# Kernel optimization log

Hardware: AMD Instinct MI355X
Metric: run time of the kernel (lower is better)

Reference implementation:

```python
import jax, jax.numpy as jnp
import numpy as np
import math

D_MODEL = 1024
N_HEADS = 16
HEAD_DIM = D_MODEL // N_HEADS
MLP_DIM = 4 * D_MODEL
B, L, M = 2, 2048, 2048


def layer_norm(x, g, b, eps=1e-5):
    mu = jnp.mean(x, axis=-1, keepdims=True)
    var = jnp.var(x, axis=-1, keepdims=True)
    return (x - mu) * jax.lax.rsqrt(var + eps) * g + b


def mha(q_in, k_in, qW, wW, oW, mask=None):
    # Faithful to source: k and v share w_proj, and the value einsum uses k.
    b, l, _ = q_in.shape
    m = k_in.shape[1]
    q = (q_in @ qW).reshape(b, l, HEAD_DIM, N_HEADS)
    k = (k_in @ wW).reshape(b, m, HEAD_DIM, N_HEADS)
    s = jnp.einsum('bldn,bmdn->blmn', q, k)
    if mask is not None:
        s = jnp.where(mask, -1e9, s)  # mask applied BEFORE scaling, as in source
    s = s / math.sqrt(HEAD_DIM)
    w = jax.nn.softmax(s, axis=2)
    x = jnp.einsum('blmn,bmdn->bldn', w, k)  # source bug: uses k, not v
    x = x.reshape(b, l, HEAD_DIM * N_HEADS)
    return x @ oW


def setup_inputs() -> dict:
    key = jax.random.key(0)
    ks = jax.random.split(key, 16)
    sc = 1.0 / math.sqrt(D_MODEL)
    inp = {
        'x': jax.random.normal(ks[0], (B, L, D_MODEL), jnp.float32),
        'enc_output': jax.random.normal(ks[1], (B, M, D_MODEL), jnp.float32),
        'mask': jax.random.randint(ks[2], (B, 1, M, 1), 0, 2).astype(bool),
        'q1W': jax.random.normal(ks[3], (D_MODEL, D_MODEL), jnp.float32) * sc,
        'w1W': jax.random.normal(ks[4], (D_MODEL, D_MODEL), jnp.float32) * sc,
        'o1W': jax.random.normal(ks[5], (D_MODEL, D_MODEL), jnp.float32) * sc,
        'q2W': jax.random.normal(ks[6], (D_MODEL, D_MODEL), jnp.float32) * sc,
        'w2W': jax.random.normal(ks[7], (D_MODEL, D_MODEL), jnp.float32) * sc,
        'o2W': jax.random.normal(ks[8], (D_MODEL, D_MODEL), jnp.float32) * sc,
        'ffW1': jax.random.normal(ks[9], (D_MODEL, MLP_DIM), jnp.float32) * sc,
        'ffb1': jnp.zeros((MLP_DIM,), jnp.float32),
        'ffW2': jax.random.normal(ks[10], (MLP_DIM, D_MODEL), jnp.float32) * sc,
        'ffb2': jnp.zeros((D_MODEL,), jnp.float32),
        'g1': jnp.ones((D_MODEL,), jnp.float32), 'b1': jnp.zeros((D_MODEL,), jnp.float32),
        'g2': jnp.ones((D_MODEL,), jnp.float32), 'b2': jnp.zeros((D_MODEL,), jnp.float32),
        'g3': jnp.ones((D_MODEL,), jnp.float32), 'b3': jnp.zeros((D_MODEL,), jnp.float32),
    }
    return inp


def reference(x, enc_output, mask, q1W, w1W, o1W, q2W, w2W, o2W,
              ffW1, ffb1, ffW2, ffb2, g1, b1, g2, b2, g3, b3):
    # self-attention (no mask, as in source)
    sa = mha(x, x, q1W, w1W, o1W, mask=None)
    x = layer_norm(x + sa, g1, b1)
    # encoder-decoder attention with mask
    ca = mha(x, enc_output, q2W, w2W, o2W, mask=mask)
    x = layer_norm(x + ca, g2, b2)
    # feed-forward (exact GELU, matching torch nn.GELU default)
    h = jax.nn.gelu(x @ ffW1 + ffb1, approximate=False)
    ff = h @ ffW2 + ffb2
    x = layer_norm(x + ff, g3, b3)
    return x
```

## Files before the change

### kernel.cpp

```cpp
#include <hip/hip_runtime.h>
#include <hip/hip_bf16.h>
#include <math.h>
#include <stdint.h>

typedef __attribute__((ext_vector_type(8))) short bf16x8_t;
typedef __attribute__((ext_vector_type(4))) float f32x4_t;

#define LOG2E 1.4426950408889634f
#define GLB(p) ((const __attribute__((address_space(1))) void*)(p))
#define LDS(p) ((__attribute__((address_space(3))) void*)(p))

__device__ __forceinline__ unsigned short f2bf(float f) {
    union { float f; unsigned int u; } v; v.f = f;
    unsigned int r = v.u + 0x7FFFu + ((v.u >> 16) & 1u);
    return (unsigned short)(r >> 16);
}

__device__ __forceinline__ float bf2f(unsigned short us) {
    union { unsigned int u; float f; } c; c.u = (unsigned int)us << 16; return c.f;
}

__device__ __forceinline__ unsigned int pack2bf(float a, float b) {
#if __has_builtin(__builtin_amdgcn_cvt_pk_bf16_f32)
    auto r = __builtin_amdgcn_cvt_pk_bf16_f32(a, b);
    unsigned int u;
    __builtin_memcpy(&u, &r, 4);
    return u;
#else
    return (unsigned int)f2bf(a) | ((unsigned int)f2bf(b) << 16);
#endif
}

__device__ __forceinline__ float fast_rcp(float x) {
#if __has_builtin(__builtin_amdgcn_rcpf)
    return __builtin_amdgcn_rcpf(x);
#else
    return 1.0f / x;
#endif
}

__device__ __forceinline__ float fexp2(float x) {
#if __has_builtin(__builtin_amdgcn_exp2f)
    return __builtin_amdgcn_exp2f(x);
#else
    return exp2f(x);
#endif
}

__device__ __forceinline__ float gelu_fast(float v) {
    float x2 = v * v;
    float inner = v * fmaf(0.0356774081f, x2, 0.7978845608f);
    inner = fminf(fmaxf(inner, -20.f), 20.f);
    float t = fexp2(inner * 2.8853900817779268f);
    return v * t * fast_rcp(t + 1.0f);
}

__global__ void cast2_bf16_k(const float* __restrict__ inA, unsigned short* __restrict__ outA,
                             const float* __restrict__ inB, unsigned short* __restrict__ outB,
                             int n4, const int* __restrict__ maskp, float* __restrict__ mask4) {
    if (blockIdx.y == 2) {
        int i = blockIdx.x * blockDim.x + threadIdx.x;
        if (i < 8192) {
            int nt = i & 3, l16 = (i >> 2) & 15, t = (i >> 6) & 31, b = (i >> 11) & 1;
            mask4[i] = maskp[b * 2048 + t * 64 + nt * 16 + l16] ? -1e10f : 0.0f;
        }
        return;
    }
    const float* in = blockIdx.y ? inB : inA;
    unsigned short* out = blockIdx.y ? outB : outA;
    int i = blockIdx.x * blockDim.x + threadIdx.x;
    if (i < n4) {
        float4 v = ((const float4*)in)[i];
        ushort4 o;
        o.x = f2bf(v.x); o.y = f2bf(v.y); o.z = f2bf(v.z); o.w = f2bf(v.w);
        ((ushort4*)out)[i] = o;
    }
}

__global__ void transpose_all_k(const float* __restrict__ s0, const float* __restrict__ s1,
                                const float* __restrict__ s2, const float* __restrict__ s3,
                                const float* __restrict__ s4, const float* __restrict__ s5,
                                const float* __restrict__ s6, const float* __restrict__ s7,
                                unsigned short* __restrict__ d0, unsigned short* __restrict__ d1,
                                unsigned short* __restrict__ d2, unsigned short* __restrict__ d3,
                                unsigned short* __restrict__ d4, unsigned short* __restrict__ d5,
                                unsigned short* __restrict__ d6, unsigned short* __restrict__ d7) {
    __shared__ float tile[32][33];
    int idx = blockIdx.x;
    const float* W; unsigned short* Wt; int K, N, bx, by;
    if (idx < 6144) {
        int which = idx >> 10, t = idx & 1023;
        bx = t & 31; by = t >> 5; K = 1024; N = 1024;
        switch (which) {
            case 0: W = s0; Wt = d0; break;
            case 1: W = s1; Wt = d1; break;
            case 2: W = s2; Wt = d2; break;
            case 3: W = s3; Wt = d3; break;
            case 4: W = s4; Wt = d4; break;
            default: W = s5; Wt = d5; break;
        }
    } else if (idx < 10240) {
        int t = idx - 6144;
        bx = t & 127; by = t >> 7; K = 1024; N = 4096;
        W = s6; Wt = d6;
    } else {
        int t = idx - 10240;
        bx = t & 31; by = t >> 5; K = 4096; N = 1024;
        W = s7; Wt = d7;
    }
    int k0 = by * 32, n0 = bx * 32;
    int tx = threadIdx.x, ty = threadIdx.y;
#pragma unroll
    for (int i = 0; i < 32; i += 8)
        tile[ty + i][tx] = W[(long)(k0 + ty + i) * N + n0 + tx];
    __syncthreads();
#pragma unroll
    for (int i = 0; i < 32; i += 8)
        Wt[(long)(n0 + ty + i) * K + k0 + tx] = f2bf(tile[tx][ty + i]);
}

template <int EP, int BN>
__global__ __launch_bounds__(256) void gemm_k(const unsigned short* __restrict__ A,
                                              const unsigned short* __restrict__ Bt,
                                              void* __restrict__ outp,
                                              const float* __restrict__ bias,
                                              int M, int N, int K) {
    __shared__ __align__(16) unsigned short As[128 * 64];
    __shared__ __align__(16) unsigned short Bs[BN * 64];
    const int NT = BN / 32;
    const int BG = BN / 32;
    int tid = threadIdx.x;
    int wave = tid >> 6, lane = tid & 63;
    int wm = wave >> 1, wn = wave & 1;
    int quad = lane >> 4, l16 = lane & 15;
    int bm = blockIdx.y * 128, bn = blockIdx.x * BN;

    f32x4_t acc[4][NT] = {};

    int srow = tid >> 3;
    int sgrp = (tid & 7) ^ (srow & 7);
    const unsigned short* Ag[4];
#pragma unroll
    for (int i = 0; i < 4; i++)
        Ag[i] = A + (long)(bm + i * 32 + srow) * K + sgrp * 8;
    const unsigned short* Bg[BG];
#pragma unroll
    for (int i = 0; i < BG; i++)
        Bg[i] = Bt + (long)(bn + i * 32 + srow) * K + sgrp * 8;

    for (int k0 = 0; k0 < K; k0 += 64) {
        __syncthreads();
#pragma unroll
        for (int i = 0; i < 4; i++)
            __builtin_amdgcn_global_load_lds(GLB(Ag[i] + k0), LDS(As + i * 2048 + tid * 8), 16, 0, 0);
#pragma unroll
        for (int i = 0; i < BG; i++)
            __builtin_amdgcn_global_load_lds(GLB(Bg[i] + k0), LDS(Bs + i * 2048 + tid * 8), 16, 0, 0);
        __syncthreads();
#pragma unroll
        for (int kk = 0; kk < 2; kk++) {
            int xg = ((kk * 4 + quad) ^ (l16 & 7)) * 8;
            bf16x8_t af[4], bfr[NT];
#pragma unroll
            for (int t = 0; t < 4; t++)
                af[t] = *(const bf16x8_t*)(As + (wm * 64 + t * 16 + l16) * 64 + xg);
#pragma unroll
            for (int t = 0; t < NT; t++)
                bfr[t] = *(const bf16x8_t*)(Bs + (wn * (BN / 2) + t * 16 + l16) * 64 + xg);
#pragma unroll
            for (int mt = 0; mt < 4; mt++)
#pragma unroll
                for (int nt = 0; nt < NT; nt++)
                    acc[mt][nt] = __builtin_amdgcn_mfma_f32_16x16x32_bf16(af[mt], bfr[nt], acc[mt][nt], 0, 0, 0);
        }
    }

#pragma unroll
    for (int mt = 0; mt < 4; mt++)
#pragma unroll
        for (int nt = 0; nt < NT; nt++)
#pragma unroll
            for (int r = 0; r < 4; r++) {
                int gm = bm + wm * 64 + mt * 16 + quad * 4 + r;
                int gn = bn + wn * (BN / 2) + nt * 16 + l16;
                float v = acc[mt][nt][r];
                if (EP == 2) {
                    v = gelu_fast(v + bias[gn]);
                    ((unsigned short*)outp)[(long)gm * N + gn] = f2bf(v);
                } else {
                    ((unsigned short*)outp)[(long)gm * N + gn] = f2bf(v);
                }
            }
}

template <int EP>
__global__ __launch_bounds__(512, 4) void gemm8_k(const unsigned short* __restrict__ A,
                                                  const unsigned short* __restrict__ Bt,
                                                  void* __restrict__ outp,
                                                  const float* __restrict__ bias,
                                                  const unsigned short* __restrict__ A2,
                                                  const unsigned short* __restrict__ Bt2,
                                                  unsigned short* __restrict__ qout,
                                                  unsigned short* __restrict__ kout,
                                                  unsigned short* __restrict__ ktout,
                                                  int M, int N, int K) {
    if (blockIdx.z) { A = A2; Bt = Bt2; }
    __shared__ __align__(16) unsigned short SMEM[32768];
    unsigned short* As = SMEM;
    unsigned short* Bs = SMEM + 16384;
    int tid = threadIdx.x;
    int wave = tid >> 6, lane = tid & 63;
    int wm = wave >> 2, wn = wave & 3;
    int quad = lane >> 4, l16 = lane & 15;
    int bm = blockIdx.y * 128, bn = blockIdx.x * 128;

    f32x4_t acc[4][2] = {};

    int srow = tid >> 3;
    int sgrp = (tid & 7) ^ (srow & 7);
    const unsigned short* Ag[2];
    const unsigned short* Bg[2];
#pragma unroll
    for (int i = 0; i < 2; i++) {
        Ag[i] = A + (long)(bm + i * 64 + srow) * K + sgrp * 8;
        Bg[i] = Bt + (long)(bn + i * 64 + srow) * K + sgrp * 8;
    }

    auto stage = [&](int buf, int k0) {
#pragma unroll
        for (int i = 0; i < 2; i++)
            __builtin_amdgcn_global_load_lds(GLB(Ag[i] + k0), LDS(As + buf * 8192 + i * 4096 + tid * 8), 16, 0, 0);
#pragma unroll
        for (int i = 0; i < 2; i++)
            __builtin_amdgcn_global_load_lds(GLB(Bg[i] + k0), LDS(Bs + buf * 8192 + i * 4096 + tid * 8), 16, 0, 0);
    };

    auto compute = [&](int buf) {
        const unsigned short* Ab = As + buf * 8192;
        const unsigned short* Bb = Bs + buf * 8192;
#pragma unroll
        for (int kk = 0; kk < 2; kk++) {
            int xg = ((kk * 4 + quad) ^ (l16 & 7)) * 8;
            bf16x8_t af[4], bfr[2];
#pragma unroll
            for (int t = 0; t < 4; t++)
                af[t] = *(const bf16x8_t*)(Ab + (wm * 64 + t * 16 + l16) * 64 + xg);
#pragma unroll
            for (int t = 0; t < 2; t++)
                bfr[t] = *(const bf16x8_t*)(Bb + (wn * 32 + t * 16 + l16) * 64 + xg);
#pragma unroll
            for (int mt = 0; mt < 4; mt++)
#pragma unroll
                for (int nt = 0; nt < 2; nt++)
                    acc[mt][nt] = __builtin_amdgcn_mfma_f32_16x16x32_bf16(af[mt], bfr[nt], acc[mt][nt], 0, 0, 0);
        }
    };

    stage(0, 0);
    const int NS = K >> 6;
    for (int i = 0; i < NS; i++) {
        if (i + 1 < NS) {
            stage((i + 1) & 1, (i + 1) << 6);
            asm volatile("s_waitcnt vmcnt(4)\n\ts_barrier" ::: "memory");
        } else {
            asm volatile("s_waitcnt vmcnt(0)\n\ts_barrier" ::: "memory");
        }
        compute(i & 1);
        asm volatile("s_barrier" ::: "memory");
    }

    if (EP == 7 || EP == 8) {
        bool kmode = (EP == 7) ? (bn >= 1024) : (blockIdx.z != 0);
        int G = (EP == 7 && kmode) ? ((bn - 1024) >> 7) : (bn >> 7);
        unsigned short* Ct = SMEM;
#pragma unroll
        for (int mt = 0; mt < 4; mt++)
#pragma unroll
            for (int nt = 0; nt < 2; nt++)
#pragma unroll
                for (int r = 0; r < 4; r++) {
                    int rr = wm * 64 + mt * 16 + quad * 4 + r;
                    int cc = wn * 32 + nt * 16 + l16;
                    Ct[rr * 132 + cc] = f2bf(acc[mt][nt][r]);
                }
        __syncthreads();
        int bq = bm >> 11;
        if (!kmode) {
#pragma unroll
            for (int i = 0; i < 4; i++) {
                int e = tid + i * 512;
                int h = e & 15, rl = e >> 4;
                int ll = (bm & 2047) + rl;
                union { uint4 v; unsigned short s[8]; } u;
#pragma unroll
                for (int j = 0; j < 8; j++) u.s[j] = Ct[rl * 132 + j * 16 + h];
                *(uint4*)(qout + (((long)(bq * 16 + h) * 2048 + ll) << 6) + ((G ^ (ll & 7)) << 3)) = u.v;
            }
        } else {
#pragma unroll
            for (int i = 0; i < 4; i++) {
                int e = tid + i * 512;
                int h = e & 15, rl = e >> 4;
                int mm = (bm & 2047) + rl;
                union { uint4 v; unsigned short s[8]; } u;
#pragma unroll
                for (int j = 0; j < 8; j++) u.s[j] = Ct[rl * 132 + j * 16 + h];
                *(uint4*)(kout + (((long)(bq * 16 + h) * 2048 + mm) << 6) + ((G ^ (mm & 7)) << 3)) = u.v;
            }
#pragma unroll
            for (int i = 0; i < 4; i++) {
                int e = tid + i * 512;
                int glog = e & 7, m0s = (e >> 3) & 1, dl = (e >> 4) & 7, h = e >> 7;
                int d = G * 8 + dl;
                union { uint4 v; unsigned short s[8]; } u;
#pragma unroll
                for (int j = 0; j < 8; j++) {
                    int p = glog * 8 + j;
                    int ml = (p >> 2) + (p & 3) * 16;
                    u.s[j] = Ct[(m0s * 64 + ml) * 132 + dl * 16 + h];
                }
                int mmbase = (bm & 2047) + m0s * 64;
                int gph = glog ^ (d & 7);
                *(uint4*)(ktout + ((long)(bq * 16 + h) * 64 + d) * 2048 + mmbase + gph * 8) = u.v;
            }
        }
        return;
    }

#pragma unroll
    for (int mt = 0; mt < 4; mt++)
#pragma unroll
        for (int nt = 0; nt < 2; nt++)
#pragma unroll
            for (int r = 0; r < 4; r++) {
                int gm = bm + wm * 64 + mt * 16 + quad * 4 + r;
                int gn = bn + wn * 32 + nt * 16 + l16;
                float v = acc[mt][nt][r];
                if (EP == 6) {
                    ((unsigned short*)outp)[(long)gm * N + gn] = f2bf(v + bias[gn]);
                } else {
                    ((unsigned short*)outp)[(long)gm * N + gn] = f2bf(v);
                }
            }
}

template <int USE_MASK>
__global__ __launch_bounds__(256, 4) void flash_attn9_k(const unsigned short* __restrict__ Qh,
                                                        const unsigned short* __restrict__ Kh,
                                                        const unsigned short* __restrict__ KhTp,
                                                        const float* __restrict__ mask4,
                                                        unsigned short* __restrict__ out) {
    __shared__ __align__(16) unsigned short K1[64 * 64];
    __shared__ __align__(16) unsigned short K2[64 * 64];
    __shared__ __align__(16) unsigned short Ps[64 * 64];
    __shared__ __align__(16) float Ml[USE_MASK ? 2048 : 4];

    int tid = threadIdx.x;
    int wave = tid >> 6, lane = tid & 63;
    int quad = lane >> 4, l16 = lane & 15;
    int bh = blockIdx.y, b = bh >> 4, h = bh & 15;
    int l0 = blockIdx.x * 64;
    const unsigned short* k1p = Kh + (long)bh * 2048 * 64 + tid * 8;
    const unsigned short* k2p = KhTp + (long)bh * 64 * 2048 + (long)(tid >> 3) * 2048 + (tid & 7) * 8;

    int sw = l16 & 7;

    const unsigned short* qrow = Qh + ((long)bh * 2048 + l0 + wave * 16 + l16) * 64;
    bf16x8_t qf[2];
#pragma unroll
    for (int kk = 0; kk < 2; kk++)
        qf[kk] = *(const bf16x8_t*)(qrow + ((kk * 4 + quad) ^ sw) * 8);

    __builtin_amdgcn_global_load_lds(GLB(k1p), LDS(K1 + tid * 8), 16, 0, 0);
    __builtin_amdgcn_global_load_lds(GLB(k1p + 2048), LDS(K1 + tid * 8 + 2048), 16, 0, 0);
    __builtin_amdgcn_global_load_lds(GLB(k2p), LDS(K2 + tid * 8), 16, 0, 0);
    __builtin_amdgcn_global_load_lds(GLB(k2p + 32 * 2048), LDS(K2 + tid * 8 + 2048), 16, 0, 0);
    if (USE_MASK) {
        const float* mp = mask4 + b * 2048;
        for (int c = tid; c < 512; c += 256)
            ((float4*)Ml)[c] = ((const float4*)mp)[c];
    }
    __syncthreads();

    const float C1 = 0.125f * LOG2E;
    f32x4_t acc_o[4] = {};
    float rs[4] = {0.f, 0.f, 0.f, 0.f};

    for (int t = 0; t < 32; ++t) {
        uint4 rA, rB, rC, rD;
        if (t < 31) {
            k1p += 4096;
            k2p += 64;
            rA = *(const uint4*)(k1p);
            rB = *(const uint4*)(k1p + 2048);
            rC = *(const uint4*)(k2p);
            rD = *(const uint4*)(k2p + 32 * 2048);
        }

        float4 mq = make_float4(0.f, 0.f, 0.f, 0.f);
        if (USE_MASK) mq = *(const float4*)(Ml + t * 64 + l16 * 4);

        f32x4_t sacc[4] = {};
        __builtin_amdgcn_s_setprio(1);
#pragma unroll
        for (int kk = 0; kk < 2; kk++) {
            int xg = ((kk * 4 + quad) ^ sw) * 8;
#pragma unroll
            for (int nt = 0; nt < 4; nt++) {
                bf16x8_t bfr = *(const bf16x8_t*)(K1 + (nt * 16 + l16) * 64 + xg);
                sacc[nt] = __builtin_amdgcn_mfma_f32_16x16x32_bf16(qf[kk], bfr, sacc[nt], 0, 0, 0);
            }
        }
        __builtin_amdgcn_s_setprio(0);

#pragma unroll
        for (int r = 0; r < 4; r++) {
            float p0 = fexp2(fmaf(sacc[0][r], C1, mq.x));
            float p1 = fexp2(fmaf(sacc[1][r], C1, mq.y));
            float p2 = fexp2(fmaf(sacc[2][r], C1, mq.z));
            float p3 = fexp2(fmaf(sacc[3][r], C1, mq.w));
            rs[r] += (p0 + p1) + (p2 + p3);
            uint2 pk; pk.x = pack2bf(p0, p1); pk.y = pack2bf(p2, p3);
            int Rrow = wave * 16 + quad * 4 + r;
            int grp = (l16 >> 1) ^ (Rrow & 7);
            *(uint2*)(Ps + Rrow * 64 + grp * 8 + (l16 & 1) * 4) = pk;
        }

        __builtin_amdgcn_s_setprio(1);
#pragma unroll
        for (int kk = 0; kk < 2; kk++) {
            int xg = ((kk * 4 + quad) ^ sw) * 8;
            int Rr = wave * 16 + l16;
            int pg = ((kk * 4 + quad) ^ (l16 & 7)) * 8;
            bf16x8_t af = *(const bf16x8_t*)(Ps + Rr * 64 + pg);
#pragma unroll
            for (int nt = 0; nt < 4; nt++) {
                bf16x8_t bfr = *(const bf16x8_t*)(K2 + (nt * 16 + l16) * 64 + xg);
                acc_o[nt] = __builtin_amdgcn_mfma_f32_16x16x32_bf16(af, bfr, acc_o[nt], 0, 0, 0);
            }
        }
        __builtin_amdgcn_s_setprio(0);

        asm volatile("s_barrier" ::: "memory");
        if (t < 31) {
            *(uint4*)(K1 + tid * 8) = rA;
            *(uint4*)(K1 + tid * 8 + 2048) = rB;
            *(uint4*)(K2 + tid * 8) = rC;
            *(uint4*)(K2 + tid * 8 + 2048) = rD;
            asm volatile("s_waitcnt lgkmcnt(0)\n\ts_barrier" ::: "memory");
        }
    }

#pragma unroll
    for (int r = 0; r < 4; r++) {
#pragma unroll
        for (int d = 1; d < 16; d <<= 1) rs[r] += __shfl_xor(rs[r], d);
    }

#pragma unroll
    for (int r = 0; r < 4; r++) {
        float inv = 1.0f / rs[r];
        int l = l0 + wave * 16 + quad * 4 + r;
#pragma unroll
        for (int nt = 0; nt < 4; nt++) {
            int d = nt * 16 + l16;
            out[((long)(b * 2048 + l)) * 1024 + d * 16 + h] = f2bf(acc_o[nt][r] * inv);
        }
    }
}

template <int AIN_BF16, int OUT_F32>
__global__ __launch_bounds__(256) void resid_ln_k(const void* __restrict__ ap,
                                                  const unsigned short* __restrict__ rb,
                                                  const float* __restrict__ g,
                                                  const float* __restrict__ bb,
                                                  float* __restrict__ outf,
                                                  unsigned short* __restrict__ outb) {
    long row = blockIdx.x;
    int tid = threadIdx.x;
    float x0, x1, x2, x3;
    if (AIN_BF16) {
        ushort4 va = ((const ushort4*)((const unsigned short*)ap + row * 1024))[tid];
        x0 = bf2f(va.x); x1 = bf2f(va.y); x2 = bf2f(va.z); x3 = bf2f(va.w);
    } else {
        float4 va = ((const float4*)((const float*)ap + row * 1024))[tid];
        x0 = va.x; x1 = va.y; x2 = va.z; x3 = va.w;
    }
    ushort4 vr = ((const ushort4*)(rb + row * 1024))[tid];
    x0 += bf2f(vr.x); x1 += bf2f(vr.y); x2 += bf2f(vr.z); x3 += bf2f(vr.w);
    float s = x0 + x1 + x2 + x3;
    float sq = x0 * x0 + x1 * x1 + x2 * x2 + x3 * x3;
#pragma unroll
    for (int d = 1; d < 64; d <<= 1) { s += __shfl_xor(s, d); sq += __shfl_xor(sq, d); }
    __shared__ float ss[4], ssq[4];
    int wave = tid >> 6, lane = tid & 63;
    if (lane == 0) { ss[wave] = s; ssq[wave] = sq; }
    __syncthreads();
    s = ss[0] + ss[1] + ss[2] + ss[3];
    sq = ssq[0] + ssq[1] + ssq[2] + ssq[3];
    float mean = s * (1.0f / 1024.0f);
    float var = sq * (1.0f / 1024.0f) - mean * mean;
    float rstd = rsqrtf(var + 1e-5f);
    float4 vg = ((const float4*)g)[tid];
    float4 vb = ((const float4*)bb)[tid];
    float y0 = (x0 - mean) * rstd * vg.x + vb.x;
    float y1 = (x1 - mean) * rstd * vg.y + vb.y;
    float y2 = (x2 - mean) * rstd * vg.z + vb.z;
    float y3 = (x3 - mean) * rstd * vg.w + vb.w;
    if (OUT_F32) {
        float4 o; o.x = y0; o.y = y1; o.z = y2; o.w = y3;
        ((float4*)(outf + row * 1024))[tid] = o;
    } else {
        ushort4 ob; ob.x = f2bf(y0); ob.y = f2bf(y1); ob.z = f2bf(y2); ob.w = f2bf(y3);
        ((ushort4*)(outb + row * 1024))[tid] = ob;
    }
}

extern "C" void kernel_launch(void* const* d_in, const int* in_sizes, int n_in,
                              void* d_out, int out_size, void* d_ws, size_t ws_size,
                              hipStream_t stream) {
    const float* x    = (const float*)d_in[0];
    const float* enc  = (const float*)d_in[1];
    const int*   mask = (const int*)d_in[2];
    const float* q1W  = (const float*)d_in[3];
    const float* w1W  = (const float*)d_in[4];
    const float* o1W  = (const float*)d_in[5];
    const float* q2W  = (const float*)d_in[6];
    const float* w2W  = (const float*)d_in[7];
    const float* o2W  = (const float*)d_in[8];
    const float* ffW1 = (const float*)d_in[9];
    const float* ffb1 = (const float*)d_in[10];
    const float* ffW2 = (const float*)d_in[11];
    const float* ffb2 = (const float*)d_in[12];
    const float* g1 = (const float*)d_in[13];
    const float* b1 = (const float*)d_in[14];
    const float* g2 = (const float*)d_in[15];
    const float* b2 = (const float*)d_in[16];
    const float* g3 = (const float*)d_in[17];
    const float* b3 = (const float*)d_in[18];
    float* outp = (float*)d_out;

    const int T = 4096;
    const int D = 1024;
    const int F = 4096;

    char* ws = (char*)d_ws;
    auto alloc = [&](size_t sz) { char* p = ws; ws += (sz + 255) & ~(size_t)255; return p; };
    unsigned short* qw1Wt = (unsigned short*)alloc((size_t)2 * D * D * 2);
    unsigned short* o1Wt  = (unsigned short*)alloc((size_t)D * D * 2);
    unsigned short* q2Wt  = (unsigned short*)alloc((size_t)D * D * 2);
    unsigned short* w2Wt  = (unsigned short*)alloc((size_t)D * D * 2);
    unsigned short* o2Wt  = (unsigned short*)alloc((size_t)D * D * 2);
    unsigned short* ffW1t = (unsigned short*)alloc((size_t)F * D * 2);
    unsigned short* ffW2t = (unsigned short*)alloc((size_t)D * F * 2);
    unsigned short* xb    = (unsigned short*)alloc((size_t)T * D * 2);
    unsigned short* encb  = (unsigned short*)alloc((size_t)T * D * 2);
    unsigned short* Qhb   = (unsigned short*)alloc((size_t)T * D * 2);
    unsigned short* Khb   = (unsigned short*)alloc((size_t)T * D * 2);
    unsigned short* KhTb  = (unsigned short*)alloc((size_t)T * D * 2);
    unsigned short* attnb = (unsigned short*)alloc((size_t)T * D * 2);
    float*          mask4b= (float*)alloc((size_t)8192 * 4);
    unsigned short* projb = (unsigned short*)alloc((size_t)T * D * 2);
    unsigned short* x1s   = (unsigned short*)alloc((size_t)T * D * 2);
    unsigned short* x2s   = (unsigned short*)alloc((size_t)T * D * 2);
    unsigned short* S1    = (unsigned short*)alloc((size_t)T * F * 2);
    unsigned short* hb    = S1;

    dim3 blk256(256);
    dim3 blk512(512);
    dim3 tblk(32, 8);

    cast2_bf16_k<<<dim3(T * D / 4 / 256, 3), blk256, 0, stream>>>(x, xb, enc, encb, T * D / 4, mask, mask4b);
    transpose_all_k<<<dim3(14336), tblk, 0, stream>>>(
        q1W, w1W, o1W, q2W, w2W, o2W, ffW1, ffW2,
        qw1Wt, qw1Wt + (size_t)D * D, o1Wt, q2Wt, w2Wt, o2Wt, ffW1t, ffW2t);

    gemm8_k<7><<<dim3(2 * D / 128, T / 128, 1), blk512, 0, stream>>>(
        xb, qw1Wt, nullptr, nullptr, nullptr, nullptr, Qhb, Khb, KhTb, T, 2 * D, D);
    flash_attn9_k<0><<<dim3(32, 32), blk256, 0, stream>>>(Qhb, Khb, KhTb, nullptr, attnb);
    gemm8_k<4><<<dim3(D / 128, T / 128, 1), blk512, 0, stream>>>(
        attnb, o1Wt, projb, nullptr, nullptr, nullptr, nullptr, nullptr, nullptr, T, D, D);
    resid_ln_k<0, 0><<<dim3(T), blk256, 0, stream>>>(x, projb, g1, b1, nullptr, x1s);

    gemm8_k<8><<<dim3(D / 128, T / 128, 2), blk512, 0, stream>>>(
        x1s, q2Wt, nullptr, nullptr, encb, w2Wt, Qhb, Khb, KhTb, T, D, D);
    flash_attn9_k<1><<<dim3(32, 32), blk256, 0, stream>>>(Qhb, Khb, KhTb, mask4b, attnb);
    gemm8_k<4><<<dim3(D / 128, T / 128, 1), blk512, 0, stream>>>(
        attnb, o2Wt, projb, nullptr, nullptr, nullptr, nullptr, nullptr, nullptr, T, D, D);
    resid_ln_k<1, 0><<<dim3(T), blk256, 0, stream>>>(x1s, projb, g2, b2, nullptr, x2s);

    gemm_k<2, 128><<<dim3(F / 128, T / 128, 1), blk256, 0, stream>>>(
        x2s, ffW1t, hb, ffb1, T, F, D);
    gemm8_k<6><<<dim3(D / 128, T / 128, 1), blk512, 0, stream>>>(
        hb, ffW2t, projb, ffb2, nullptr, nullptr, nullptr, nullptr, nullptr, T, D, F);
    resid_ln_k<1, 1><<<dim3(T), blk256, 0, stream>>>(x2s, projb, g3, b3, outp, nullptr);
}
```

Measured before the change: 490.7 us.

## Template gemm8 on tile width, add grid swizzle, route FFN1 through pipelined kernel

Adds a BN template parameter to the double-buffered gemm8 kernel so the N=1024 projections and FFN2 use 128x64 tiles, doubling block count for better CU occupancy. Adds an XCD-aware block index swizzle that groups consecutive blocks onto the same die for L2 reuse. Replaces the single-buffered gemm_k used by FFN1 with the pipelined gemm8 path, including GELU epilogue. Smaller tiles lower per-block arithmetic intensity and the swizzle assumes grid size divisible by 8.

```diff
diff --git a/kernel.cpp b/kernel.cpp
--- a/kernel.cpp
+++ b/kernel.cpp
@@ -120,80 +120,6 @@
 }
 
 template <int EP, int BN>
-__global__ __launch_bounds__(256) void gemm_k(const unsigned short* __restrict__ A,
-                                              const unsigned short* __restrict__ Bt,
-                                              void* __restrict__ outp,
-                                              const float* __restrict__ bias,
-                                              int M, int N, int K) {
-    __shared__ __align__(16) unsigned short As[128 * 64];
-    __shared__ __align__(16) unsigned short Bs[BN * 64];
-    const int NT = BN / 32;
-    const int BG = BN / 32;
-    int tid = threadIdx.x;
-    int wave = tid >> 6, lane = tid & 63;
-    int wm = wave >> 1, wn = wave & 1;
-    int quad = lane >> 4, l16 = lane & 15;
-    int bm = blockIdx.y * 128, bn = blockIdx.x * BN;
-
-    f32x4_t acc[4][NT] = {};
-
-    int srow = tid >> 3;
-    int sgrp = (tid & 7) ^ (srow & 7);
-    const unsigned short* Ag[4];
-#pragma unroll
-    for (int i = 0; i < 4; i++)
-        Ag[i] = A + (long)(bm + i * 32 + srow) * K + sgrp * 8;
-    const unsigned short* Bg[BG];
-#pragma unroll
-    for (int i = 0; i < BG; i++)
-        Bg[i] = Bt + (long)(bn + i * 32 + srow) * K + sgrp * 8;
-
-    for (int k0 = 0; k0 < K; k0 += 64) {
-        __syncthreads();
-#pragma unroll
-        for (int i = 0; i < 4; i++)
-            __builtin_amdgcn_global_load_lds(GLB(Ag[i] + k0), LDS(As + i * 2048 + tid * 8), 16, 0, 0);
-#pragma unroll
-        for (int i = 0; i < BG; i++)
-            __builtin_amdgcn_global_load_lds(GLB(Bg[i] + k0), LDS(Bs + i * 2048 + tid * 8), 16, 0, 0);
-        __syncthreads();
-#pragma unroll
-        for (int kk = 0; kk < 2; kk++) {
-            int xg = ((kk * 4 + quad) ^ (l16 & 7)) * 8;
-            bf16x8_t af[4], bfr[NT];
-#pragma unroll
-            for (int t = 0; t < 4; t++)
-                af[t] = *(const bf16x8_t*)(As + (wm * 64 + t * 16 + l16) * 64 + xg);
-#pragma unroll
-            for (int t = 0; t < NT; t++)
-                bfr[t] = *(const bf16x8_t*)(Bs + (wn * (BN / 2) + t * 16 + l16) * 64 + xg);
-#pragma unroll
-            for (int mt = 0; mt < 4; mt++)
-#pragma unroll
-                for (int nt = 0; nt < NT; nt++)
-                    acc[mt][nt] = __builtin_amdgcn_mfma_f32_16x16x32_bf16(af[mt], bfr[nt], acc[mt][nt], 0, 0, 0);
-        }
-    }
-
-#pragma unroll
-    for (int mt = 0; mt < 4; mt++)
-#pragma unroll
-        for (int nt = 0; nt < NT; nt++)
-#pragma unroll
-            for (int r = 0; r < 4; r++) {
-                int gm = bm + wm * 64 + mt * 16 + quad * 4 + r;
-                int gn = bn + wn * (BN / 2) + nt * 16 + l16;
-                float v = acc[mt][nt][r];
-                if (EP == 2) {
-                    v = gelu_fast(v + bias[gn]);
-                    ((unsigned short*)outp)[(long)gm * N + gn] = f2bf(v);
-                } else {
-                    ((unsigned short*)outp)[(long)gm * N + gn] = f2bf(v);
-                }
-            }
-}
-
-template <int EP>
 __global__ __launch_bounds__(512, 4) void gemm8_k(const unsigned short* __restrict__ A,
                                                   const unsigned short* __restrict__ Bt,
                                                   void* __restrict__ outp,
@@ -205,51 +131,62 @@
                                                   unsigned short* __restrict__ ktout,
                                                   int M, int N, int K) {
     if (blockIdx.z) { A = A2; Bt = Bt2; }
-    __shared__ __align__(16) unsigned short SMEM[32768];
+    constexpr int WN = (BN == 128) ? 4 : 2;
+    constexpr int WM = 8 / WN;
+    constexpr int MT = 128 / WM / 16;
+    constexpr int BG = BN / 64;
+    __shared__ __align__(16) unsigned short SMEM[16384 + BN * 128];
     unsigned short* As = SMEM;
     unsigned short* Bs = SMEM + 16384;
     int tid = threadIdx.x;
     int wave = tid >> 6, lane = tid & 63;
-    int wm = wave >> 2, wn = wave & 3;
+    int wm = wave / WN, wn = wave % WN;
     int quad = lane >> 4, l16 = lane & 15;
-    int bm = blockIdx.y * 128, bn = blockIdx.x * 128;
-
-    f32x4_t acc[4][2] = {};
+
+    int gx = gridDim.x, gyd = gridDim.y;
+    int o = blockIdx.y * gx + blockIdx.x;
+    int cpx = (gx * gyd) >> 3;
+    int sz = (o & 7) * cpx + (o >> 3);
+    int bxi = sz / gyd, byi = sz - bxi * gyd;
+    int bm = byi * 128, bn = bxi * BN;
+
+    f32x4_t acc[MT][2] = {};
 
     int srow = tid >> 3;
     int sgrp = (tid & 7) ^ (srow & 7);
     const unsigned short* Ag[2];
-    const unsigned short* Bg[2];
-#pragma unroll
-    for (int i = 0; i < 2; i++) {
+    const unsigned short* Bg[BG];
+#pragma unroll
+    for (int i = 0; i < 2; i++)
         Ag[i] = A + (long)(bm + i * 64 + srow) * K + sgrp * 8;
+#pragma unroll
+    for (int i = 0; i < BG; i++)
         Bg[i] = Bt + (long)(bn + i * 64 + srow) * K + sgrp * 8;
-    }
 
     auto stage = [&](int buf, int k0) {
 #pragma unroll
         for (int i = 0; i < 2; i++)
             __builtin_amdgcn_global_load_lds(GLB(Ag[i] + k0), LDS(As + buf * 8192 + i * 4096 + tid * 8), 16, 0, 0);
 #pragma unroll
-        for (int i = 0; i < 2; i++)
-            __builtin_amdgcn_global_load_lds(GLB(Bg[i] + k0), LDS(Bs + buf * 8192 + i * 4096 + tid * 8), 16, 0, 0);
+        for (int i = 0; i < BG; i++)
+            __builtin_amdgcn_global_load_lds(GLB(Bg[i] + k0), LDS(Bs + buf * (BN * 64) + i * 4096 + tid * 8), 16, 0, 0);
     };
 
     auto compute = [&](int buf) {
         const unsigned short* Ab = As + buf * 8192;
-        const unsigned short* Bb = Bs + buf * 8192;
+        const unsigned short* Bb = Bs + buf * (BN * 64);
 #pragma unroll
         for (int kk = 0; kk < 2; kk++) {
             int xg = ((kk * 4 + quad) ^ (l16 & 7)) * 8;
-            bf16x8_t af[4], bfr[2];
-#pragma unroll
-            for (int t = 0; t < 4; t++)
-                af[t] = *(const bf16x8_t*)(Ab + (wm * 64 + t * 16 + l16) * 64 + xg);
+            bf16x8_t af[MT], bfr[2];
+#pragma unroll
+            for (int t = 0; t < MT; t++)
+                af[t] = *(const bf16x8_t*)(Ab + (wm * (MT * 16) + t * 16 + l16) * 64 + xg);
 #pragma unroll
             for (int t = 0; t < 2; t++)
                 bfr[t] = *(const bf16x8_t*)(Bb + (wn * 32 + t * 16 + l16) * 64 + xg);
 #pragma unroll
-            for (int mt = 0; mt < 4; mt++)
+            for (int mt = 0; mt < MT; mt++)
 #pragma unroll
                 for (int nt = 0; nt < 2; nt++)
                     acc[mt][nt] = __builtin_amdgcn_mfma_f32_16x16x32_bf16(af[mt], bfr[nt], acc[mt][nt], 0, 0, 0);
@@ -261,7 +198,10 @@
     for (int i = 0; i < NS; i++) {
         if (i + 1 < NS) {
             stage((i + 1) & 1, (i + 1) << 6);
-            asm volatile("s_waitcnt vmcnt(4)\n\ts_barrier" ::: "memory");
+            if constexpr (BN == 128)
+                asm volatile("s_waitcnt vmcnt(4)\n\ts_barrier" ::: "memory");
+            else
+                asm volatile("s_waitcnt vmcnt(3)\n\ts_barrier" ::: "memory");
         } else {
             asm volatile("s_waitcnt vmcnt(0)\n\ts_barrier" ::: "memory");
         }
@@ -274,12 +214,12 @@
         int G = (EP == 7 && kmode) ? ((bn - 1024) >> 7) : (bn >> 7);
         unsigned short* Ct = SMEM;
 #pragma unroll
-        for (int mt = 0; mt < 4; mt++)
+        for (int mt = 0; mt < MT; mt++)
 #pragma unroll
             for (int nt = 0; nt < 2; nt++)
 #pragma unroll
                 for (int r = 0; r < 4; r++) {
-                    int rr = wm * 64 + mt * 16 + quad * 4 + r;
+                    int rr = wm * (MT * 16) + mt * 16 + quad * 4 + r;
                     int cc = wn * 32 + nt * 16 + l16;
                     Ct[rr * 132 + cc] = f2bf(acc[mt][nt][r]);
                 }
@@ -328,15 +268,18 @@
     }
 
 #pragma unroll
-    for (int mt = 0; mt < 4; mt++)
+    for (int mt = 0; mt < MT; mt++)
 #pragma unroll
         for (int nt = 0; nt < 2; nt++)
 #pragma unroll
             for (int r = 0; r < 4; r++) {
-                int gm = bm + wm * 64 + mt * 16 + quad * 4 + r;
+                int gm = bm + wm * (MT * 16) + mt * 16 + quad * 4 + r;
                 int gn = bn + wn * 32 + nt * 16 + l16;
                 float v = acc[mt][nt][r];
-                if (EP == 6) {
+                if (EP == 2) {
+                    v = gelu_fast(v + bias[gn]);
+                    ((unsigned short*)outp)[(long)gm * N + gn] = f2bf(v);
+                } else if (EP == 6) {
                     ((unsigned short*)outp)[(long)gm * N + gn] = f2bf(v + bias[gn]);
                 } else {
                     ((unsigned short*)outp)[(long)gm * N + gn] = f2bf(v);
@@ -575,23 +518,23 @@
         q1W, w1W, o1W, q2W, w2W, o2W, ffW1, ffW2,
         qw1Wt, qw1Wt + (size_t)D * D, o1Wt, q2Wt, w2Wt, o2Wt, ffW1t, ffW2t);
 
-    gemm8_k<7><<<dim3(2 * D / 128, T / 128, 1), blk512, 0, stream>>>(
+    gemm8_k<7, 128><<<dim3(2 * D / 128, T / 128, 1), blk512, 0, stream>>>(
         xb, qw1Wt, nullptr, nullptr, nullptr, nullptr, Qhb, Khb, KhTb, T, 2 * D, D);
     flash_attn9_k<0><<<dim3(32, 32), blk256, 0, stream>>>(Qhb, Khb, KhTb, nullptr, attnb);
-    gemm8_k<4><<<dim3(D / 128, T / 128, 1), blk512, 0, stream>>>(
+    gemm8_k<4, 64><<<dim3(D / 64, T / 128, 1), blk512, 0, stream>>>(
         attnb, o1Wt, projb, nullptr, nullptr, nullptr, nullptr, nullptr, nullptr, T, D, D);
     resid_ln_k<0, 0><<<dim3(T), blk256, 0, stream>>>(x, projb, g1, b1, nullptr, x1s);
 
-    gemm8_k<8><<<dim3(D / 128, T / 128, 2), blk512, 0, stream>>>(
+    gemm8_k<8, 128><<<dim3(D / 128, T / 128, 2), blk512, 0, stream>>>(
         x1s, q2Wt, nullptr, nullptr, encb, w2Wt, Qhb, Khb, KhTb, T, D, D);
     flash_attn9_k<1><<<dim3(32, 32), blk256, 0, stream>>>(Qhb, Khb, KhTb, mask4b, attnb);
-    gemm8_k<4><<<dim3(D / 128, T / 128, 1), blk512, 0, stream>>>(
+    gemm8_k<4, 64><<<dim3(D / 64, T / 128, 1), blk512, 0, stream>>>(
         attnb, o2Wt, projb, nullptr, nullptr, nullptr, nullptr, nullptr, nullptr, T, D, D);
     resid_ln_k<1, 0><<<dim3(T), blk256, 0, stream>>>(x1s, projb, g2, b2, nullptr, x2s);
 
-    gemm_k<2, 128><<<dim3(F / 128, T / 128, 1), blk256, 0, stream>>>(
-        x2s, ffW1t, hb, ffb1, T, F, D);
-    gemm8_k<6><<<dim3(D / 128, T / 128, 1), blk512, 0, stream>>>(
+    gemm8_k<2, 128><<<dim3(F / 128, T / 128, 1), blk512, 0, stream>>>(
+        x2s, ffW1t, hb, ffb1, nullptr, nullptr, nullptr, nullptr, nullptr, T, F, D);
+    gemm8_k<6, 64><<<dim3(D / 64, T / 128, 1), blk512, 0, stream>>>(
         hb, ffW2t, projb, ffb2, nullptr, nullptr, nullptr, nullptr, nullptr, T, D, F);
     resid_ln_k<1, 1><<<dim3(T), blk256, 0, stream>>>(x2s, projb, g3, b3, outp, nullptr);
 }
```

New measurement: 512.1 us. +4.4%, slower.
